# Optimization experiments

Measured on AMD Instinct MI355X. Metric: run time of the kernel, lower is better.

Reference implementation:

```python
import jax, jax.numpy as jnp
import numpy as np

N, E = 50000, 800000
IN, OUT = 128, 64
NEG_SLOPE = 0.2


def setup_inputs() -> dict:
    key = jax.random.key(0)
    ks = jax.random.split(key, 8)
    x = jax.random.normal(ks[0], (N, IN), dtype=jnp.float32)
    edge_index = jax.random.randint(ks[1], (2, E), 0, N, dtype=jnp.int64)
    s_in = 1.0 / np.sqrt(IN)
    s_out = 1.0 / np.sqrt(OUT)
    Wl = jax.random.normal(ks[2], (OUT, IN), dtype=jnp.float32) * s_in   # lin_l weight
    bl = jax.random.normal(ks[3], (OUT,), dtype=jnp.float32) * s_in     # lin_l bias
    Wr = jax.random.normal(ks[4], (OUT, IN), dtype=jnp.float32) * s_in  # lin_r weight
    br = jax.random.normal(ks[5], (OUT,), dtype=jnp.float32) * s_in     # lin_r bias
    att = jax.random.normal(ks[6], (OUT,), dtype=jnp.float32) * s_out   # attention vector a
    bias = jnp.zeros((OUT,), dtype=jnp.float32)                          # final output bias
    return dict(x=x, Wl=Wl, bl=bl, Wr=Wr, br=br, att=att, bias=bias, edge_index=edge_index)


def reference(x, Wl, bl, Wr, br, att, bias, edge_index):
    n = x.shape[0]
    loop = jnp.arange(n, dtype=edge_index.dtype)
    src = jnp.concatenate([edge_index[0], loop])  # add_self_loops=True
    dst = jnp.concatenate([edge_index[1], loop])
    xl = x @ Wl.T + bl  # [N, OUT] source transform (x_j)
    xr = x @ Wr.T + br  # [N, OUT] target transform (x_i)
    h = xl[src] + xr[dst]                              # [E+N, OUT]
    h = jnp.where(h > 0, h, NEG_SLOPE * h)             # LeakyReLU(0.2)
    e = h @ att                                        # [E+N] edge logits
    # segment softmax over destination nodes (every node has a self-loop)
    m = jax.ops.segment_max(e, dst, num_segments=n)
    ex = jnp.exp(e - m[dst])
    s = jax.ops.segment_sum(ex, dst, num_segments=n)
    alpha = ex / s[dst]
    out = jax.ops.segment_sum(alpha[:, None] * xl[src], dst, num_segments=n) + bias
    return jax.nn.relu(out)  # norm=Identity, dropout inactive at inference
```

## Files before the change

### kernel.cpp

```cpp
#include <hip/hip_runtime.h>
#include <hip/hip_bf16.h>

#define NEG_SLOPE 0.2f
#define CAP 5120
#define CHUNK 4096
#define LOG2E 1.4426950408889634f

typedef __attribute__((ext_vector_type(8))) short short8v;
typedef __attribute__((ext_vector_type(4))) short short4v;
typedef __attribute__((ext_vector_type(4))) float f32x4;
typedef _Float16 __attribute__((ext_vector_type(8))) h8;
typedef _Float16 __attribute__((ext_vector_type(2))) h2;

__device__ __forceinline__ short f2bf(float f) {
  __hip_bfloat16 b = __float2bfloat16(f);
  return *reinterpret_cast<short*>(&b);
}

__device__ __forceinline__ float dot8f(h8 a, h8 b, float c) {
#if __has_builtin(__builtin_amdgcn_fdot2)
  c = __builtin_amdgcn_fdot2(__builtin_shufflevector(a, a, 0, 1),
                             __builtin_shufflevector(b, b, 0, 1), c, false);
  c = __builtin_amdgcn_fdot2(__builtin_shufflevector(a, a, 2, 3),
                             __builtin_shufflevector(b, b, 2, 3), c, false);
  c = __builtin_amdgcn_fdot2(__builtin_shufflevector(a, a, 4, 5),
                             __builtin_shufflevector(b, b, 4, 5), c, false);
  c = __builtin_amdgcn_fdot2(__builtin_shufflevector(a, a, 6, 7),
                             __builtin_shufflevector(b, b, 6, 7), c, false);
#else
#pragma unroll
  for (int i = 0; i < 8; ++i) c += (float)a[i] * (float)b[i];
#endif
  return c;
}

__device__ __forceinline__ h8 leaky8(h8 hs) {
  h8 hl = hs * (_Float16)NEG_SLOPE;
  return __builtin_elementwise_max(hs, hl);
}

__device__ __forceinline__ h8 shfl_xor_h8(h8 v, int off) {
  int4 i = *(int4*)&v;
  i.x = __shfl_xor(i.x, off);
  i.y = __shfl_xor(i.y, off);
  i.z = __shfl_xor(i.z, off);
  i.w = __shfl_xor(i.w, off);
  return *(h8*)&i;
}

__device__ __forceinline__ float row_reduce8(float p) {
  p += __int_as_float(__builtin_amdgcn_update_dpp(
      0, __float_as_int(p), 0xB1, 0xF, 0xF, true));
  p += __int_as_float(__builtin_amdgcn_update_dpp(
      0, __float_as_int(p), 0x4E, 0xF, 0xF, true));
  p += __int_as_float(__builtin_amdgcn_update_dpp(
      0, __float_as_int(p), 0x141, 0xF, 0xF, true));
  return p;
}

__global__ __launch_bounds__(256) void k_prep(
    const float* __restrict__ Wl, const float* __restrict__ Wr,
    const float* __restrict__ bl, const float* __restrict__ br,
    short* __restrict__ W2, float* __restrict__ biasc,
    int* __restrict__ bcur, int nbk) {
  int idx = blockIdx.x * 256 + threadIdx.x;
  if (idx < 128 * 128) {
    int j = idx >> 7, k = idx & 127;
    float v = (j < 64) ? Wl[j * 128 + k] : Wr[(j - 64) * 128 + k];
    W2[idx] = f2bf(v);
  } else {
    int z = idx - 128 * 128;
    if (z < nbk) bcur[z] = 0;
  }
  if (idx < 128) biasc[idx] = (idx < 64) ? bl[idx] : br[idx - 64];
}

__global__ __launch_bounds__(256) void k_tbf(
    const float* __restrict__ x, const short* __restrict__ W2,
    const float* __restrict__ biasc, const int* __restrict__ eidx,
    int* __restrict__ bcur, unsigned* __restrict__ pk,
    _Float16* __restrict__ xlh, _Float16* __restrict__ xrh, int nN, int E_,
    int nbf) {
  __shared__ union {
    struct { int hist[256]; int base[256]; } bf;
    short xs[64 * 136];
  } u;
  const int t = threadIdx.x;

  if (blockIdx.x < nbf) {
    u.bf.hist[t] = 0;
    __syncthreads();
    const int e0 = blockIdx.x * CHUNK + t * 16;
    unsigned mypk[16];
    int myrank[16];
    const bool valid = (e0 < E_);
    if (valid) {
      const int4* ps = (const int4*)(eidx + e0);
      const int4* pd = (const int4*)(eidx + E_ + e0);
#pragma unroll
      for (int j = 0; j < 4; ++j) {
        int4 sv = ps[j];
        int4 dv = pd[j];
        int ss[4] = {sv.x, sv.y, sv.z, sv.w};
        int dd[4] = {dv.x, dv.y, dv.z, dv.w};
#pragma unroll
        for (int q = 0; q < 4; ++q) {
          unsigned p = ((unsigned)dd[q] << 16) | (unsigned)ss[q];
          mypk[j * 4 + q] = p;
          myrank[j * 4 + q] = atomicAdd(&u.bf.hist[dd[q] >> 8], 1);
        }
      }
    }
    __syncthreads();
    u.bf.base[t] = u.bf.hist[t] ? atomicAdd(&bcur[t], u.bf.hist[t]) : 0;
    __syncthreads();
    if (valid) {
#pragma unroll
      for (int j = 0; j < 16; ++j) {
        int b = mypk[j] >> 24;
        unsigned idx = (unsigned)(u.bf.base[b] + myrank[j]);
        if (idx < CAP) pk[(unsigned)b * CAP + idx] = mypk[j];
      }
    }
    return;
  }

  const int n0 = (blockIdx.x - nbf) * 64;
#pragma unroll
  for (int i = 0; i < 8; ++i) {
    int f = (i * 256 + t) * 4;
    int node = f >> 7, k = f & 127;
    int gn = min(n0 + node, nN - 1);
    float4 v = *(const float4*)(x + (size_t)gn * 128 + k);
    short4v s4;
    s4[0] = f2bf(v.x); s4[1] = f2bf(v.y); s4[2] = f2bf(v.z); s4[3] = f2bf(v.w);
    *(short4v*)(u.xs + node * 136 + k) = s4;
  }
  __syncthreads();

  const int w = t >> 6;
  const int lane = t & 63;
  const int r = lane & 15;
  const int kb = lane >> 4;

  short8v bfr[2][4];
#pragma unroll
  for (int c = 0; c < 2; ++c) {
    const short* bp = W2 + (size_t)((w * 2 + c) * 16 + r) * 128 + kb * 8;
#pragma unroll
    for (int kk = 0; kk < 4; ++kk) bfr[c][kk] = *(const short8v*)(bp + kk * 32);
  }

  f32x4 acc[4][2];
#pragma unroll
  for (int nt = 0; nt < 4; ++nt)
#pragma unroll
    for (int c = 0; c < 2; ++c) acc[nt][c] = (f32x4){0.f, 0.f, 0.f, 0.f};

#pragma unroll
  for (int nt = 0; nt < 4; ++nt) {
    short8v afr[4];
#pragma unroll
    for (int kk = 0; kk < 4; ++kk)
      afr[kk] =
          *(const short8v*)(u.xs + (nt * 16 + r) * 136 + kb * 8 + kk * 32);
#pragma unroll
    for (int kk = 0; kk < 4; ++kk) {
      acc[nt][0] =
          __builtin_amdgcn_mfma_f32_16x16x32_bf16(afr[kk], bfr[0][kk],
                                                  acc[nt][0], 0, 0, 0);
      acc[nt][1] =
          __builtin_amdgcn_mfma_f32_16x16x32_bf16(afr[kk], bfr[1][kk],
                                                  acc[nt][1], 0, 0, 0);
    }
  }

#pragma unroll
  for (int c = 0; c < 2; ++c) {
    const int ch = (w * 2 + c) * 16 + r;
    const float bv = biasc[ch];
#pragma unroll
    for (int nt = 0; nt < 4; ++nt) {
#pragma unroll
      for (int i = 0; i < 4; ++i) {
        int node = n0 + nt * 16 + kb * 4 + i;
        if (node < nN) {
          float v = acc[nt][c][i] + bv;
          if (ch < 64) xlh[(size_t)node * 64 + ch] = (_Float16)v;
          else         xrh[(size_t)node * 64 + (ch - 64)] = (_Float16)v;
        }
      }
    }
  }
}

__global__ __launch_bounds__(256) void k_nfill(
    const unsigned* __restrict__ pk, const int* __restrict__ bcur,
    int* __restrict__ rowlo, int* __restrict__ rowhi,
    unsigned short* __restrict__ csr, int nN) {
  __shared__ int hist[256];
  __shared__ int nbase[256];
  __shared__ int wsum[4];
  const int b = blockIdx.x;
  const int t = threadIdx.x;
  const int nb0 = b << 8;
  const int cnt = min(bcur[b], CAP);
  const unsigned gbase = (unsigned)b * CAP;
  hist[t] = 0;
  __syncthreads();
  for (int i = t; i < cnt; i += 256)
    atomicAdd(&hist[(pk[gbase + i] >> 16) & 255], 1);
  __syncthreads();
  const int lane = t & 63;
  const int wid = t >> 6;
  int v = hist[t];
  const int orig = v;
#pragma unroll
  for (int off = 1; off < 64; off <<= 1) {
    int uu = __shfl_up(v, off);
    if (lane >= off) v += uu;
  }
  if (lane == 63) wsum[wid] = v;
  __syncthreads();
  int add = 0;
  for (int ww = 0; ww < wid; ++ww) add += wsum[ww];
  const int excl = v - orig + add;
  nbase[t] = excl;
  if (nb0 + t < nN) {
    rowlo[nb0 + t] = (int)gbase + excl;
    rowhi[nb0 + t] = (int)gbase + excl + orig;
  }
  __syncthreads();
  hist[t] = 0;
  __syncthreads();
  for (int i = t; i < cnt; i += 256) {
    unsigned p = pk[gbase + i];
    int dl = (p >> 16) & 255;
    int slot = nbase[dl] + atomicAdd(&hist[dl], 1);
    csr[gbase + slot] = (unsigned short)(p & 0xFFFFu);
  }
}

__global__ __launch_bounds__(256) void k_node(
    const int* __restrict__ rowlo, const int* __restrict__ rowhi,
    const unsigned short* __restrict__ csr, const _Float16* __restrict__ xlh,
    const _Float16* __restrict__ xrh, const float* __restrict__ att,
    const float* __restrict__ bias, float* __restrict__ out, int nN) {
  const int wvid = (blockIdx.x * 256 + threadIdx.x) >> 6;
  const int lane = threadIdx.x & 63;
  const int h = lane >> 5;
  const int g = (lane >> 3) & 3;
  const int r = lane & 7;
  int d = wvid * 2 + h;
  if (wvid * 2 >= nN) return;
  const bool live = (d < nN);
  d = min(d, nN - 1);

  h8 at8;
#pragma unroll
  for (int i = 0; i < 8; ++i) at8[i] = (_Float16)att[r * 8 + i];

  const h8 xr8 = *(const h8*)(xrh + (size_t)d * 64 + r * 8);
  const h8 sv8 = *(const h8*)(xlh + (size_t)d * 64 + r * 8);

  float ps = dot8f(leaky8(sv8 + xr8), at8, 0.f);
  ps = row_reduce8(ps) * LOG2E;

  const bool g0 = (g == 0);
  float m = ps;
  float ssum = g0 ? 1.f : 0.f;
  h8 acc = g0 ? sv8 : (h8){0, 0, 0, 0, 0, 0, 0, 0};

  const int lo = live ? rowlo[d] : 0;
  const int hi = live ? rowhi[d] : 0;
  const int nst = (hi - lo + 3) >> 2;

#define PROC(VREG, SIDX)                                                      \
  {                                                                           \
    const bool act = ((SIDX) < hi);                                           \
    float p = dot8f(leaky8(VREG + xr8), at8, 0.f);                            \
    p = row_reduce8(p);                                                       \
    const float pm = act ? p * LOG2E : -3.0e38f;                              \
    if (__any(pm > m)) {             \
      float q = pm;                                                           \
      q = fmaxf(q, __shfl_xor(q, 8));                                         \
      q = fmaxf(q, __shfl_xor(q, 16));                     \
      const float nm = fmaxf(m, q);                     \
      const float sc = exp2f(m - nm);                                         \
      const float w = exp2f(pm - nm);                                         \
      ssum = fmaf(ssum, sc, w);                                               \
      acc = acc * (_Float16)sc + VREG * (_Float16)w;                          \
      m = nm;                                                                 \
    } else {                                  \
      const float w = exp2f(pm - m);                                          \
      ssum += w;                                                              \
      acc += VREG * (_Float16)w;                                              \
    }                                                                         \
  }

  int sA = lo + g, sB = sA + 4, sC = sA + 8;
  h8 vA, vB, vC;
  {
    int srcA = (sA < hi) ? (int)csr[sA] : d;
    vA = *(const h8*)(xlh + (size_t)srcA * 64 + r * 8);
    int srcB = (sB < hi) ? (int)csr[sB] : d;
    vB = *(const h8*)(xlh + (size_t)srcB * 64 + r * 8);
    int srcC = (sC < hi) ? (int)csr[sC] : d;
    vC = *(const h8*)(xlh + (size_t)srcC * 64 + r * 8);
  }

  int tt = 0;
  for (; tt + 2 < nst; tt += 3) {
    PROC(vA, sA);
    if (tt + 3 < nst) {
      int sN = sA + 12;
      int srcN = (sN < hi) ? (int)csr[sN] : d;
      vA = *(const h8*)(xlh + (size_t)srcN * 64 + r * 8);
    }
    PROC(vB, sB);
    if (tt + 4 < nst) {
      int sN = sB + 12;
      int srcN = (sN < hi) ? (int)csr[sN] : d;
      vB = *(const h8*)(xlh + (size_t)srcN * 64 + r * 8);
    }
    PROC(vC, sC);
    if (tt + 5 < nst) {
      int sN = sC + 12;
      int srcN = (sN < hi) ? (int)csr[sN] : d;
      vC = *(const h8*)(xlh + (size_t)srcN * 64 + r * 8);
    }
    sA += 12; sB += 12; sC += 12;
  }
  {
    const int rem = nst - tt;
    if (rem > 0) PROC(vA, sA);
    if (rem > 1) PROC(vB, sB);
  }
#undef PROC

#pragma unroll
  for (int off = 8; off <= 16; off <<= 1) {
    ssum += __shfl_xor(ssum, off);
    acc += shfl_xor_h8(acc, off);
  }

  if (g0 && live) {
    const float inv = 1.0f / ssum;
    const float4 bA = *(const float4*)(bias + r * 8);
    const float4 bB = *(const float4*)(bias + r * 8 + 4);
    float4 oA, oB;
    oA.x = fmaxf(fmaf((float)acc[0], inv, bA.x), 0.f);
    oA.y = fmaxf(fmaf((float)acc[1], inv, bA.y), 0.f);
    oA.z = fmaxf(fmaf((float)acc[2], inv, bA.z), 0.f);
    oA.w = fmaxf(fmaf((float)acc[3], inv, bA.w), 0.f);
    oB.x = fmaxf(fmaf((float)acc[4], inv, bB.x), 0.f);
    oB.y = fmaxf(fmaf((float)acc[5], inv, bB.y), 0.f);
    oB.z = fmaxf(fmaf((float)acc[6], inv, bB.z), 0.f);
    oB.w = fmaxf(fmaf((float)acc[7], inv, bB.w), 0.f);
    *(float4*)(out + (size_t)d * 64 + r * 8) = oA;
    *(float4*)(out + (size_t)d * 64 + r * 8 + 4) = oB;
  }
}

extern "C" void kernel_launch(void* const* d_in, const int* in_sizes, int n_in,
                              void* d_out, int out_size, void* d_ws,
                              size_t ws_size, hipStream_t stream) {
  const float* x    = (const float*)d_in[0];
  const float* Wl   = (const float*)d_in[1];
  const float* bl   = (const float*)d_in[2];
  const float* Wr   = (const float*)d_in[3];
  const float* br   = (const float*)d_in[4];
  const float* att  = (const float*)d_in[5];
  const float* bias = (const float*)d_in[6];
  const int* eidx   = (const int*)d_in[7];
  float* out = (float*)d_out;

  const int N = in_sizes[0] / 128;
  const int E = in_sizes[7] / 2;
  const int NB = (N + 255) >> 8;
  const int nbf = (E + CHUNK - 1) / CHUNK;
  const int ntr = (N + 63) / 64;

  _Float16* xlh = (_Float16*)d_ws;
  _Float16* xrh = xlh + (size_t)N * 64;
  unsigned* pk = (unsigned*)(xrh + (size_t)N * 64);
  unsigned short* csr = (unsigned short*)(pk + (size_t)NB * CAP);
  short* W2    = (short*)(csr + (size_t)NB * CAP);
  float* biasc = (float*)(W2 + 128 * 128);
  int* bcur    = (int*)(biasc + 128);
  int* rowlo   = bcur + NB;
  int* rowhi   = rowlo + N;

  k_prep<<<(128 * 128 + NB + 255) / 256, 256, 0, stream>>>(
      Wl, Wr, bl, br, W2, biasc, bcur, NB);
  k_tbf<<<nbf + ntr, 256, 0, stream>>>(x, W2, biasc, eidx, bcur, pk, xlh, xrh,
                                       N, E, nbf);
  k_nfill<<<NB, 256, 0, stream>>>(pk, bcur, rowlo, rowhi, csr, N);
  {
    int waves = (N + 1) / 2;
    k_node<<<(waves + 3) / 4, 256, 0, stream>>>(rowlo, rowhi, csr, xlh, xrh,
                                                att, bias, out, N);
  }
}
```

Before: 69.29 us.

## Drop prep kernel, sort nodes by degree for wave pairing, deepen gather prefetch

Removes the weight-packing prep kernel: k_tbf now converts Wl/Wr to bf16 and reads the biases inline, and bcur is zeroed with a memset. This saves one launch. k_nfill now ranks the 256 nodes of each bucket by degree and emits a permutation, so each wave handles two nodes of similar degree. That is meant to cut divergence between the two half-waves. The node kernel's gather pipeline goes from 3 to 4 in-flight rows per lane group, which adds register pressure and an O(256) rank loop per block.

```diff
diff --git a/kernel.cpp b/kernel.cpp
--- a/kernel.cpp
+++ b/kernel.cpp
@@ -58,26 +58,10 @@
   return p;
 }
 
-__global__ __launch_bounds__(256) void k_prep(
-    const float* __restrict__ Wl, const float* __restrict__ Wr,
-    const float* __restrict__ bl, const float* __restrict__ br,
-    short* __restrict__ W2, float* __restrict__ biasc,
-    int* __restrict__ bcur, int nbk) {
-  int idx = blockIdx.x * 256 + threadIdx.x;
-  if (idx < 128 * 128) {
-    int j = idx >> 7, k = idx & 127;
-    float v = (j < 64) ? Wl[j * 128 + k] : Wr[(j - 64) * 128 + k];
-    W2[idx] = f2bf(v);
-  } else {
-    int z = idx - 128 * 128;
-    if (z < nbk) bcur[z] = 0;
-  }
-  if (idx < 128) biasc[idx] = (idx < 64) ? bl[idx] : br[idx - 64];
-}
-
 __global__ __launch_bounds__(256) void k_tbf(
-    const float* __restrict__ x, const short* __restrict__ W2,
-    const float* __restrict__ biasc, const int* __restrict__ eidx,
+    const float* __restrict__ x, const float* __restrict__ Wl,
+    const float* __restrict__ Wr, const float* __restrict__ bl,
+    const float* __restrict__ br, const int* __restrict__ eidx,
     int* __restrict__ bcur, unsigned* __restrict__ pk,
     _Float16* __restrict__ xlh, _Float16* __restrict__ xrh, int nN, int E_,
     int nbf) {
@@ -146,9 +130,18 @@
   short8v bfr[2][4];
 #pragma unroll
   for (int c = 0; c < 2; ++c) {
-    const short* bp = W2 + (size_t)((w * 2 + c) * 16 + r) * 128 + kb * 8;
-#pragma unroll
-    for (int kk = 0; kk < 4; ++kk) bfr[c][kk] = *(const short8v*)(bp + kk * 32);
+    const int ch = (w * 2 + c) * 16 + r;
+    const float* wrow = ((ch < 64) ? (Wl + (size_t)ch * 128)
+                                   : (Wr + (size_t)(ch - 64) * 128)) + kb * 8;
+#pragma unroll
+    for (int kk = 0; kk < 4; ++kk) {
+      float4 w0 = *(const float4*)(wrow + kk * 32);
+      float4 w1 = *(const float4*)(wrow + kk * 32 + 4);
+      short8v b;
+      b[0] = f2bf(w0.x); b[1] = f2bf(w0.y); b[2] = f2bf(w0.z); b[3] = f2bf(w0.w);
+      b[4] = f2bf(w1.x); b[5] = f2bf(w1.y); b[6] = f2bf(w1.z); b[7] = f2bf(w1.w);
+      bfr[c][kk] = b;
+    }
   }
 
   f32x4 acc[4][2];
@@ -178,7 +171,7 @@
 #pragma unroll
   for (int c = 0; c < 2; ++c) {
     const int ch = (w * 2 + c) * 16 + r;
-    const float bv = biasc[ch];
+    const float bv = (ch < 64) ? bl[ch] : br[ch - 64];
 #pragma unroll
     for (int nt = 0; nt < 4; ++nt) {
 #pragma unroll
@@ -197,14 +190,17 @@
 __global__ __launch_bounds__(256) void k_nfill(
     const unsigned* __restrict__ pk, const int* __restrict__ bcur,
     int* __restrict__ rowlo, int* __restrict__ rowhi,
-    unsigned short* __restrict__ csr, int nN) {
+    unsigned short* __restrict__ csr, unsigned* __restrict__ nperm, int nN) {
   __shared__ int hist[256];
   __shared__ int nbase[256];
   __shared__ int wsum[4];
+  __shared__ int keys[256];
+  __shared__ int sortedi[256];
   const int b = blockIdx.x;
   const int t = threadIdx.x;
   const int nb0 = b << 8;
   const int cnt = min(bcur[b], CAP);
+  const int cntN = min(256, nN - nb0);
   const unsigned gbase = (unsigned)b * CAP;
   hist[t] = 0;
   __syncthreads();
@@ -226,35 +222,53 @@
   for (int ww = 0; ww < wid; ++ww) add += wsum[ww];
   const int excl = v - orig + add;
   nbase[t] = excl;
-  if (nb0 + t < nN) {
+  if (t < cntN) {
     rowlo[nb0 + t] = (int)gbase + excl;
     rowhi[nb0 + t] = (int)gbase + excl + orig;
   }
   __syncthreads();
   hist[t] = 0;
-  __syncthreads();
+  keys[t] = ((t < cntN ? orig : -1) << 8) | t;
+  __syncthreads();
+  {
+    const int mykey = keys[t];
+    int rank = 0;
+    for (int i = 0; i < 256; ++i) rank += (keys[i] > mykey);
+    sortedi[rank] = t;
+  }
   for (int i = t; i < cnt; i += 256) {
     unsigned p = pk[gbase + i];
     int dl = (p >> 16) & 255;
     int slot = nbase[dl] + atomicAdd(&hist[dl], 1);
     csr[gbase + slot] = (unsigned short)(p & 0xFFFFu);
   }
+  __syncthreads();
+  if (t < 128) {
+    int loc0 = sortedi[2 * t], loc1 = sortedi[2 * t + 1];
+    unsigned pr;
+    if (loc0 >= cntN) pr = 0xFFFFFFFFu;
+    else pr = ((unsigned)loc0 << 16) |
+              (loc1 < cntN ? (unsigned)loc1 : 0xFFFFu);
+    nperm[b * 128 + t] = pr;
+  }
 }
 
 __global__ __launch_bounds__(256) void k_node(
-    const int* __restrict__ rowlo, const int* __restrict__ rowhi,
-    const unsigned short* __restrict__ csr, const _Float16* __restrict__ xlh,
-    const _Float16* __restrict__ xrh, const float* __restrict__ att,
-    const float* __restrict__ bias, float* __restrict__ out, int nN) {
+    const unsigned* __restrict__ nperm, const int* __restrict__ rowlo,
+    const int* __restrict__ rowhi, const unsigned short* __restrict__ csr,
+    const _Float16* __restrict__ xlh, const _Float16* __restrict__ xrh,
+    const float* __restrict__ att, const float* __restrict__ bias,
+    float* __restrict__ out, int nN) {
   const int wvid = (blockIdx.x * 256 + threadIdx.x) >> 6;
+  const unsigned pr = nperm[wvid];
+  if (pr == 0xFFFFFFFFu) return;
   const int lane = threadIdx.x & 63;
   const int h = lane >> 5;
   const int g = (lane >> 3) & 3;
   const int r = lane & 7;
-  int d = wvid * 2 + h;
-  if (wvid * 2 >= nN) return;
-  const bool live = (d < nN);
-  d = min(d, nN - 1);
+  const unsigned loc = h ? (pr & 0xFFFFu) : (pr >> 16);
+  const bool live = (loc != 0xFFFFu);
+  const int d = ((wvid >> 7) << 8) + (live ? (int)loc : 0);
 
   h8 at8;
 #pragma unroll
@@ -281,7 +295,7 @@
     float p = dot8f(leaky8(VREG + xr8), at8, 0.f);                            \
     p = row_reduce8(p);                                                       \
     const float pm = act ? p * LOG2E : -3.0e38f;                              \
-    if (__any(pm > m)) {             \
+    if (__any(pm > m)) {                   \
       float q = pm;                                                           \
       q = fmaxf(q, __shfl_xor(q, 8));                                         \
       q = fmaxf(q, __shfl_xor(q, 16));                     \
@@ -298,8 +312,8 @@
     }                                                                         \
   }
 
-  int sA = lo + g, sB = sA + 4, sC = sA + 8;
-  h8 vA, vB, vC;
+  int sA = lo + g, sB = sA + 4, sC = sA + 8, sD = sA + 12;
+  h8 vA, vB, vC, vD;
   {
     int srcA = (sA < hi) ? (int)csr[sA] : d;
     vA = *(const h8*)(xlh + (size_t)srcA * 64 + r * 8);
@@ -307,34 +321,43 @@
     vB = *(const h8*)(xlh + (size_t)srcB * 64 + r * 8);
     int srcC = (sC < hi) ? (int)csr[sC] : d;
     vC = *(const h8*)(xlh + (size_t)srcC * 64 + r * 8);
+    int srcD = (sD < hi) ? (int)csr[sD] : d;
+    vD = *(const h8*)(xlh + (size_t)srcD * 64 + r * 8);
   }
 
   int tt = 0;
-  for (; tt + 2 < nst; tt += 3) {
+  for (; tt + 3 < nst; tt += 4) {
     PROC(vA, sA);
-    if (tt + 3 < nst) {
-      int sN = sA + 12;
+    if (tt + 4 < nst) {
+      int sN = sA + 16;
       int srcN = (sN < hi) ? (int)csr[sN] : d;
       vA = *(const h8*)(xlh + (size_t)srcN * 64 + r * 8);
     }
     PROC(vB, sB);
-    if (tt + 4 < nst) {
-      int sN = sB + 12;
+    if (tt + 5 < nst) {
+      int sN = sB + 16;
       int srcN = (sN < hi) ? (int)csr[sN] : d;
       vB = *(const h8*)(xlh + (size_t)srcN * 64 + r * 8);
     }
     PROC(vC, sC);
-    if (tt + 5 < nst) {
-      int sN = sC + 12;
+    if (tt + 6 < nst) {
+      int sN = sC + 16;
       int srcN = (sN < hi) ? (int)csr[sN] : d;
       vC = *(const h8*)(xlh + (size_t)srcN * 64 + r * 8);
     }
-    sA += 12; sB += 12; sC += 12;
+    PROC(vD, sD);
+    if (tt + 7 < nst) {
+      int sN = sD + 16;
+      int srcN = (sN < hi) ? (int)csr[sN] : d;
+      vD = *(const h8*)(xlh + (size_t)srcN * 64 + r * 8);
+    }
+    sA += 16; sB += 16; sC += 16; sD += 16;
   }
   {
     const int rem = nst - tt;
     if (rem > 0) PROC(vA, sA);
     if (rem > 1) PROC(vB, sB);
+    if (rem > 2) PROC(vC, sC);
   }
 #undef PROC
 
@@ -385,20 +408,15 @@
   _Float16* xrh = xlh + (size_t)N * 64;
   unsigned* pk = (unsigned*)(xrh + (size_t)N * 64);
   unsigned short* csr = (unsigned short*)(pk + (size_t)NB * CAP);
-  short* W2    = (short*)(csr + (size_t)NB * CAP);
-  float* biasc = (float*)(W2 + 128 * 128);
-  int* bcur    = (int*)(biasc + 128);
+  int* bcur    = (int*)(csr + (size_t)NB * CAP);
   int* rowlo   = bcur + NB;
   int* rowhi   = rowlo + N;
-
-  k_prep<<<(128 * 128 + NB + 255) / 256, 256, 0, stream>>>(
-      Wl, Wr, bl, br, W2, biasc, bcur, NB);
-  k_tbf<<<nbf + ntr, 256, 0, stream>>>(x, W2, biasc, eidx, bcur, pk, xlh, xrh,
-                                       N, E, nbf);
-  k_nfill<<<NB, 256, 0, stream>>>(pk, bcur, rowlo, rowhi, csr, N);
-  {
-    int waves = (N + 1) / 2;
-    k_node<<<(waves + 3) / 4, 256, 0, stream>>>(rowlo, rowhi, csr, xlh, xrh,
-                                                att, bias, out, N);
-  }
-}
+  unsigned* nperm = (unsigned*)(rowhi + N);
+
+  hipMemsetAsync(bcur, 0, (size_t)NB * sizeof(int), stream);
+  k_tbf<<<nbf + ntr, 256, 0, stream>>>(x, Wl, Wr, bl, br, eidx, bcur, pk, xlh,
+                                       xrh, N, E, nbf);
+  k_nfill<<<NB, 256, 0, stream>>>(pk, bcur, rowlo, rowhi, csr, nperm, N);
+  k_node<<<NB * 32, 256, 0, stream>>>(nperm, rowlo, rowhi, csr, xlh, xrh, att,
+                                      bias, out, N);
+}
```

After: 79.80 us. 1.15x slower.
